# Kernel optimization log

Measured on AMD Instinct MI355X. Metric: run time of the kernel, lower is better.

Reference implementation:

```python
import jax, jax.numpy as jnp
import numpy as np

N_NODES = 50000
N_EDGES = 1600000
IN_DIM = 128
HID = 64
EPS = 1e-6


def setup_inputs() -> dict:
    key = jax.random.key(0)
    ks = jax.random.split(key, 12)
    def g(k, shape, scale):
        return jax.random.normal(k, shape, dtype=jnp.float32) * scale
    x = g(ks[0], (N_NODES, IN_DIM), 1.0)
    edge_index = jax.random.randint(ks[1], (2, N_EDGES), 0, N_NODES, dtype=jnp.int64)
    return {
        "x": x,
        "edge_index": edge_index,
        "w0s": g(ks[2], (IN_DIM, HID), 1.0 / np.sqrt(IN_DIM)),
        "w0n": g(ks[3], (IN_DIM, HID), 1.0 / np.sqrt(IN_DIM)),
        "w1s": g(ks[4], (HID, HID), 1.0 / np.sqrt(HID)),
        "w1n": g(ks[5], (HID, HID), 1.0 / np.sqrt(HID)),
        "w2s": g(ks[6], (HID, HID), 1.0 / np.sqrt(HID)),
        "w2n": g(ks[7], (HID, HID), 1.0 / np.sqrt(HID)),
        "mw1": g(ks[8], (HID, 32), 1.0 / np.sqrt(HID)),
        "mb1": jnp.zeros((32,), jnp.float32),
        "mw2": g(ks[9], (32, 1), 1.0 / np.sqrt(32.0)),
        "mb2": jnp.zeros((1,), jnp.float32),
    }


def _uhg_layer(h, src, dst, inv_deg, ws, wn):
    # transform-then-gather (cheaper: GEMM at node granularity, gather at edge granularity)
    msg = (h @ wn)[src]                                    # [E, HID]
    agg = jax.ops.segment_sum(msg, dst, num_segments=N_NODES) * inv_deg  # mean over in-neighbors
    h2 = jax.nn.relu(h @ ws + agg)
    # projective (UHG) normalization: map embedding back onto the unit sphere / projective rep
    return h2 / (jnp.linalg.norm(h2, axis=-1, keepdims=True) + EPS)


def reference(x, edge_index, w0s, w0n, w1s, w1n, w2s, w2n, mw1, mb1, mw2, mb2):
    src, dst = edge_index[0], edge_index[1]
    deg = jax.ops.segment_sum(jnp.ones((N_EDGES,), jnp.float32), dst, num_segments=N_NODES)
    inv_deg = (1.0 / jnp.maximum(deg, 1.0))[:, None]       # [N,1]
    h = _uhg_layer(x, src, dst, inv_deg, w0s, w0n)
    h = _uhg_layer(h, src, dst, inv_deg, w1s, w1n)
    h = _uhg_layer(h, src, dst, inv_deg, w2s, w2n)
    h = jax.nn.relu(h @ mw1 + mb1)                         # [N,32]
    return jax.nn.sigmoid(h @ mw2 + mb2)                   # [N,1]
```

## Files before the change

### kernel.cpp

```cpp
#include <hip/hip_runtime.h>
#include <hip/hip_bf16.h>
#include <math.h>

#define N_NODES 50000
#define N_EDGES 1600000
#define IN_DIM  128
#define HID     64
#define EPB     4096
#define NBLK    391
#define NB      391
#define CAP     8192
#define PBKT    8192
static constexpr float EPS = 1e-6f;

typedef __attribute__((ext_vector_type(8))) short          short8;
typedef __attribute__((ext_vector_type(8))) unsigned short ushort8;
typedef __attribute__((ext_vector_type(4))) unsigned short bf16x4_t;
typedef __attribute__((ext_vector_type(4))) int            i32x4;
typedef __attribute__((ext_vector_type(4))) float          f32x4;
typedef __attribute__((ext_vector_type(2))) float          f32x2;

__device__ __forceinline__ unsigned short f2bf(float f) {
    union { float f; unsigned int i; } c; c.f = f;
    unsigned int r = c.i + 0x7FFFu + ((c.i >> 16) & 1u);
    return (unsigned short)(r >> 16);
}
__device__ __forceinline__ unsigned char f2fp8(float f) {
    int p = __builtin_amdgcn_cvt_pk_fp8_f32(f, f, 0, false);
    return (unsigned char)(p & 0xff);
}


template <int K>
__device__ __forceinline__ void pack_body(const float* __restrict__ wS,
                                          const float* __restrict__ wN,
                                          unsigned short* __restrict__ pS,
                                          unsigned short* __restrict__ pN, int blk) {
    constexpr int NSLOT = (K / 32) * 4 * 64;
    int slot = blk * 256 + (int)threadIdx.x;
    if (slot >= NSLOT) return;
    int lane = slot & 63;
    int ct   = slot >> 6;
    int t    = ct & 3;
    int c    = ct >> 2;
    int m    = lane & 15;
    int quad = lane >> 4;
    int col  = t * 16 + m;
#pragma unroll
    for (int j = 0; j < 8; ++j) {
        int k = c * 32 + quad * 8 + j;
        pS[slot * 8 + j] = f2bf(wS[k * 64 + col]);
        pN[slot * 8 + j] = f2bf(wN[k * 64 + col]);
    }
}


__global__ __launch_bounds__(256) void bucket_count_pack(
    const int* __restrict__ ei, int* __restrict__ blockCounts,
    const float* __restrict__ w0s, const float* __restrict__ w0n,
    const float* __restrict__ w1s, const float* __restrict__ w1n,
    const float* __restrict__ w2s, const float* __restrict__ w2n,
    unsigned short* __restrict__ p0S, unsigned short* __restrict__ p0N,
    unsigned short* __restrict__ p1S, unsigned short* __restrict__ p1N,
    unsigned short* __restrict__ p2S, unsigned short* __restrict__ p2N,
    unsigned char* __restrict__ hnqA, unsigned char* __restrict__ hnqB) {
    if (blockIdx.x >= NBLK) {
        int blk = blockIdx.x - NBLK;
        if (blk == 7) {
            if (threadIdx.x >= 128 && threadIdx.x < 144)
                ((unsigned int*)(hnqA + (size_t)N_NODES * HID))[threadIdx.x - 128] = 0u;
            if (threadIdx.x >= 144 && threadIdx.x < 160)
                ((unsigned int*)(hnqB + (size_t)N_NODES * HID))[threadIdx.x - 144] = 0u;
        }
        if (blk < 4)      pack_body<IN_DIM>(w0s, w0n, p0S, p0N, blk);
        else if (blk < 6) pack_body<HID>(w1s, w1n, p1S, p1N, blk - 4);
        else              pack_body<HID>(w2s, w2n, p2S, p2N, blk - 6);
        return;
    }
    __shared__ int hist[NB];
    for (int i = threadIdx.x; i < NB; i += 256) hist[i] = 0;
    __syncthreads();
    int base = blockIdx.x * EPB;
    int lim  = min(EPB, N_EDGES - base);
    for (int i = threadIdx.x; i < lim; i += 256)
        atomicAdd(&hist[ei[N_EDGES + base + i] >> 7], 1);
    __syncthreads();
    for (int b = threadIdx.x; b < NB; b += 256)
        blockCounts[blockIdx.x * NB + b] = hist[b];
}

template <int K, bool F32IN>
__device__ __forceinline__ void gemm_body(
    const void* __restrict__ Av,
    const unsigned short* __restrict__ pS,
    const unsigned short* __restrict__ pN,
    float* __restrict__ hs, unsigned char* __restrict__ hnq, int blk) {
    constexpr int NC = K / 32;
    int lane = threadIdx.x & 63;
    int wv   = threadIdx.x >> 6;
    int tile = blk * 4 + wv;
    if (tile >= N_NODES / 16) return;
    int m    = lane & 15;
    int quad = lane >> 4;

    const short8* pSf = (const short8*)pS;
    const short8* pNf = (const short8*)pN;

    f32x4 accS[4], accN[4];
#pragma unroll
    for (int t = 0; t < 4; ++t) {
        accS[t] = (f32x4){0.f, 0.f, 0.f, 0.f};
        accN[t] = (f32x4){0.f, 0.f, 0.f, 0.f};
    }
#pragma unroll
    for (int c = 0; c < NC; ++c) {
        short8 a;
        if constexpr (F32IN) {
            const float* Af = (const float*)Av + ((size_t)tile * 16 + m) * K + quad * 8 + c * 32;
            f32x4 a0 = *(const f32x4*)Af;
            f32x4 a1 = *(const f32x4*)(Af + 4);
#pragma unroll
            for (int k = 0; k < 4; ++k) a[k]     = (short)f2bf(a0[k]);
#pragma unroll
            for (int k = 0; k < 4; ++k) a[k + 4] = (short)f2bf(a1[k]);
        } else {
            const short8* Af = (const short8*)((const unsigned short*)Av +
                               ((size_t)tile * 16 + m) * K + quad * 8);
            a = Af[c * 4];
        }
#pragma unroll
        for (int t = 0; t < 4; ++t) {
            short8 bs = pSf[(c * 4 + t) * 64 + lane];
            short8 bn = pNf[(c * 4 + t) * 64 + lane];
            accS[t] = __builtin_amdgcn_mfma_f32_16x16x32_bf16(a, bs, accS[t], 0, 0, 0);
            accN[t] = __builtin_amdgcn_mfma_f32_16x16x32_bf16(a, bn, accN[t], 0, 0, 0);
        }
    }
    int row0 = tile * 16 + quad * 4;
#pragma unroll
    for (int t = 0; t < 4; ++t) {
#pragma unroll
        for (int r = 0; r < 4; ++r) {
            size_t o = (size_t)(row0 + r) * HID + t * 16 + m;
            hs[o]  = accS[t][r];
            hnq[o] = f2fp8(accN[t][r]);
        }
    }
}

__global__ __launch_bounds__(256) void col_sum_gemm0(
    const int* __restrict__ blockCounts, int* __restrict__ totals,
    const float* __restrict__ x,
    const unsigned short* __restrict__ p0S, const unsigned short* __restrict__ p0N,
    float* __restrict__ hs, unsigned char* __restrict__ hnq) {
    if (blockIdx.x >= NB) {
        gemm_body<IN_DIM, true>(x, p0S, p0N, hs, hnq, blockIdx.x - NB);
        return;
    }
    __shared__ int ws[4];
    int b = blockIdx.x;
    int s = 0;
    for (int i = threadIdx.x; i < NBLK; i += 256) s += blockCounts[i * NB + b];
#pragma unroll
    for (int off = 32; off >= 1; off >>= 1) s += __shfl_xor(s, off, 64);
    if ((threadIdx.x & 63) == 0) ws[threadIdx.x >> 6] = s;
    __syncthreads();
    if (threadIdx.x == 0) totals[b] = ws[0] + ws[1] + ws[2] + ws[3];
}

__global__ __launch_bounds__(256) void col_fix_base(int* __restrict__ blockCounts,
                                                    const int* __restrict__ totals,
                                                    int* __restrict__ bucketBase) {
    __shared__ int vals[NBLK];
    __shared__ int sbase;
    int b = blockIdx.x;
    for (int i = threadIdx.x; i < NBLK; i += 256) vals[i] = blockCounts[i * NB + b];
    if (threadIdx.x < 64) {
        int lane = threadIdx.x;
        int s = 0;
        for (int i = lane; i < b; i += 64) s += totals[i];
#pragma unroll
        for (int off = 32; off >= 1; off >>= 1) s += __shfl_xor(s, off, 64);
        if (lane == 0) {
            sbase = s;
            bucketBase[b] = s;
            if (b == NB - 1) bucketBase[NB] = s + totals[b];
        }
    }
    __syncthreads();
    if (threadIdx.x < 64) {
        int lane  = threadIdx.x;
        int carry = sbase;
        for (int base = 0; base < NBLK; base += 64) {
            int i = base + lane;
            int v = (i < NBLK) ? vals[i] : 0;
            int incl = v;
#pragma unroll
            for (int off = 1; off < 64; off <<= 1) {
                int t = __shfl_up(incl, off, 64);
                if (lane >= off) incl += t;
            }
            if (i < NBLK) vals[i] = carry + incl - v;
            carry += __shfl(incl, 63, 64);
        }
    }
    __syncthreads();
    for (int i = threadIdx.x; i < NBLK; i += 256) blockCounts[i * NB + b] = vals[i];
}

__global__ __launch_bounds__(256) void bucket_scatter(const int* __restrict__ ei,
                                                      const int* __restrict__ blockCounts,
                                                      unsigned int* __restrict__ bucketPacked) {
    __shared__ int cur[NB];
    for (int b = threadIdx.x; b < NB; b += 256)
        cur[b] = blockCounts[blockIdx.x * NB + b];
    __syncthreads();
    int base = blockIdx.x * EPB;
    int lim  = min(EPB, N_EDGES - base);
    for (int i = threadIdx.x; i < lim; i += 256) {
        int s = ei[base + i];
        int d = ei[N_EDGES + base + i];
        int pos = atomicAdd(&cur[d >> 7], 1);
        bucketPacked[pos] = ((unsigned int)s << 7) | (unsigned int)(d & 127);
    }
}

__global__ __launch_bounds__(256) void node_scan_scatter_pad(
    const unsigned int* __restrict__ bucketPacked, const int* __restrict__ bucketBase,
    int* __restrict__ pbeg, int* __restrict__ rdeg, int* __restrict__ csr_pad) {
    __shared__ int cnt[128];
    __shared__ int half0;
    __shared__ unsigned int stage[CAP];
    int tid = threadIdx.x;
    if (tid < 128) cnt[tid] = 0;
    __syncthreads();
    int beg = bucketBase[blockIdx.x], end = bucketBase[blockIdx.x + 1];
    int n = end - beg;
    for (int i = tid; i < n; i += 256) {
        unsigned int e = bucketPacked[beg + i];
        if (i < CAP) stage[i] = e;
        atomicAdd(&cnt[e & 127], 1);
    }
    __syncthreads();
    int lane = tid & 63;
    int v    = (tid < 128) ? cnt[tid] : 0;
    int vp   = (v + 7) & ~7;
    int incl = vp;
#pragma unroll
    for (int off = 1; off < 64; off <<= 1) {
        int t = __shfl_up(incl, off, 64);
        if (lane >= off) incl += t;
    }
    if (tid == 63) half0 = incl;
    __syncthreads();
    int start = blockIdx.x * PBKT + ((tid >= 64 && tid < 128) ? half0 : 0) + incl - vp;
    int node  = blockIdx.x * 128 + tid;
    if (tid < 128 && node < N_NODES) {
        pbeg[node] = start;
        rdeg[node] = v;
        for (int j = v; j < vp; ++j) csr_pad[start + j] = N_NODES;
        cnt[tid] = start;
    }
    __syncthreads();
    for (int i = tid; i < n; i += 256) {
        unsigned int e = (i < CAP) ? stage[i] : bucketPacked[beg + i];
        int pos = atomicAdd(&cnt[e & 127], 1);
        csr_pad[pos] = (int)(e >> 7);
    }
}

template <bool MLP>
__global__ __launch_bounds__(256) void agg_update(
    const int* __restrict__ pbeg, const int* __restrict__ rdeg,
    const int* __restrict__ csr_pad,
    const unsigned char* __restrict__ hnq, const float* __restrict__ hs,
    const unsigned short* __restrict__ pS, const unsigned short* __restrict__ pN,
    float* __restrict__ hs2, unsigned char* __restrict__ hnq2,
    const float* __restrict__ mw1, const float* __restrict__ mb1,
    const float* __restrict__ mw2, const float* __restrict__ mb2,
    float* __restrict__ out) {
    __shared__ unsigned short sA[MLP ? 1 : 16 * 80];
    __shared__ float sW1[MLP ? HID * 32 : 1];
    __shared__ float sW2[MLP ? 32 : 1];
    __shared__ float sB1[MLP ? 32 : 1];
    __shared__ float sH[MLP ? 16 * 68 : 1];
    if (MLP) {
        for (int i = threadIdx.x; i < HID * 32; i += 256) sW1[i] = mw1[i];
        if (threadIdx.x < 32) { sW2[threadIdx.x] = mw2[threadIdx.x]; sB1[threadIdx.x] = mb1[threadIdx.x]; }
        __syncthreads();
    }
    int sn   = threadIdx.x >> 4;
    int r    = threadIdx.x & 15;
    int node = blockIdx.x * 16 + sn;
    int beg  = pbeg[node];
    int dg   = rdeg[node];
    int nbat = (dg + 7) >> 3;
    const i32x4* ip = (const i32x4*)(csr_pad + beg);
    unsigned r4 = (unsigned)(r * 4);

    f32x2 acc2[2];
    acc2[0] = (f32x2){0.f, 0.f};
    acc2[1] = (f32x2){0.f, 0.f};

#pragma unroll 2
    for (int t = 0; t < nbat; ++t) {
        i32x4 a = ip[2 * t];
        i32x4 b = ip[2 * t + 1];
        unsigned wv[8];
#pragma unroll
        for (int u = 0; u < 4; ++u)
            wv[u]     = *(const unsigned*)(hnq + (((unsigned)a[u] << 6) + r4));
#pragma unroll
        for (int u = 0; u < 4; ++u)
            wv[u + 4] = *(const unsigned*)(hnq + (((unsigned)b[u] << 6) + r4));
#pragma unroll
        for (int u = 0; u < 8; ++u) {
#if __has_builtin(__builtin_amdgcn_cvt_pk_f32_fp8)
            acc2[0] += __builtin_amdgcn_cvt_pk_f32_fp8((int)wv[u], false);
            acc2[1] += __builtin_amdgcn_cvt_pk_f32_fp8((int)wv[u], true);
#else
            acc2[0] += (f32x2){__builtin_amdgcn_cvt_f32_fp8((int)wv[u], 0),
                               __builtin_amdgcn_cvt_f32_fp8((int)wv[u], 1)};
            acc2[1] += (f32x2){__builtin_amdgcn_cvt_f32_fp8((int)wv[u], 2),
                               __builtin_amdgcn_cvt_f32_fp8((int)wv[u], 3)};
#endif
        }
    }

    float acc[4] = {acc2[0][0], acc2[0][1], acc2[1][0], acc2[1][1]};
    float invdeg = 1.0f / fmaxf((float)dg, 1.0f);
    f32x4 h = *(const f32x4*)(hs + (size_t)node * HID + r * 4);
    float v[4], ss = 0.f;
#pragma unroll
    for (int k = 0; k < 4; ++k) {
        v[k] = fmaxf(fmaf(acc[k], invdeg, h[k]), 0.f);
        ss += v[k] * v[k];
    }
    ss += __shfl_xor(ss, 1, 64);
    ss += __shfl_xor(ss, 2, 64);
    ss += __shfl_xor(ss, 4, 64);
    ss += __shfl_xor(ss, 8, 64);
    float rs = 1.0f / (sqrtf(ss) + EPS);

    if constexpr (!MLP) {
        unsigned short* ap = &sA[sn * 80 + r * 4];
#pragma unroll
        for (int k = 0; k < 4; ++k) ap[k] = f2bf(v[k] * rs);
        __syncthreads();
        int lane = threadIdx.x & 63;
        int wv_  = threadIdx.x >> 6;
        int m    = lane & 15;
        int quad = lane >> 4;
        const short8* pB = (const short8*)((wv_ < 2) ? pS : pN);
        int t0 = (wv_ & 1) * 2;
        f32x4 gacc[2];
        gacc[0] = (f32x4){0.f, 0.f, 0.f, 0.f};
        gacc[1] = (f32x4){0.f, 0.f, 0.f, 0.f};
#pragma unroll
        for (int c = 0; c < 2; ++c) {
            short8 a = *(const short8*)&sA[m * 80 + quad * 8 + c * 32];
#pragma unroll
            for (int tt = 0; tt < 2; ++tt) {
                short8 b = pB[(c * 4 + t0 + tt) * 64 + lane];
                gacc[tt] = __builtin_amdgcn_mfma_f32_16x16x32_bf16(a, b, gacc[tt], 0, 0, 0);
            }
        }
        int row0 = blockIdx.x * 16 + quad * 4;
#pragma unroll
        for (int tt = 0; tt < 2; ++tt) {
            int col = (t0 + tt) * 16 + m;
#pragma unroll
            for (int rr = 0; rr < 4; ++rr) {
                size_t o = (size_t)(row0 + rr) * HID + col;
                if (wv_ < 2) hs2[o]  = gacc[tt][rr];
                else         hnq2[o] = f2fp8(gacc[tt][rr]);
            }
        }
    } else {
#pragma unroll
        for (int k = 0; k < 4; ++k) sH[sn * 68 + r * 4 + k] = v[k] * rs;
        __syncthreads();
        int c0 = r * 2;
        float y0 = sB1[c0], y1 = sB1[c0 + 1];
        const float* hrow2 = &sH[sn * 68];
#pragma unroll 8
        for (int k = 0; k < HID; ++k) {
            float hv = hrow2[k];
            y0 = fmaf(hv, sW1[k * 32 + c0], y0);
            y1 = fmaf(hv, sW1[k * 32 + c0 + 1], y1);
        }
        float p = fmaxf(y0, 0.f) * sW2[c0] + fmaxf(y1, 0.f) * sW2[c0 + 1];
        p += __shfl_xor(p, 1, 64);
        p += __shfl_xor(p, 2, 64);
        p += __shfl_xor(p, 4, 64);
        p += __shfl_xor(p, 8, 64);
        if (r == 0) out[node] = 1.0f / (1.0f + __expf(-(p + mb2[0])));
    }
}

extern "C" void kernel_launch(void* const* d_in, const int* in_sizes, int n_in,
                              void* d_out, int out_size, void* d_ws, size_t ws_size,
                              hipStream_t stream) {
    const float* x   = (const float*)d_in[0];
    const int*   ei  = (const int*)d_in[1];
    const float* w0s = (const float*)d_in[2];
    const float* w0n = (const float*)d_in[3];
    const float* w1s = (const float*)d_in[4];
    const float* w1n = (const float*)d_in[5];
    const float* w2s = (const float*)d_in[6];
    const float* w2n = (const float*)d_in[7];
    const float* mw1 = (const float*)d_in[8];
    const float* mb1 = (const float*)d_in[9];
    const float* mw2 = (const float*)d_in[10];
    const float* mb2 = (const float*)d_in[11];
    float*       out = (float*)d_out;

    int* pbeg        = (int*)d_ws;
    int* rdeg        = pbeg + 50048;
    int* blockCounts = rdeg + 50048;
    int* bucketBase  = blockCounts + 153600;
    int* totals      = bucketBase + 512;
    unsigned int* bucketPacked = (unsigned int*)(totals + 512);
    int* csr_pad     = (int*)(bucketPacked + N_EDGES);
    const size_t NH = (size_t)N_NODES * HID;
    float*          hsA  = (float*)(csr_pad + NB * PBKT);
    unsigned char*  hnqA = (unsigned char*)(hsA + NH);
    float*          hsB  = (float*)(hnqA + NH + 64);
    unsigned char*  hnqB = (unsigned char*)(hsB + NH);
    unsigned short* p0S = (unsigned short*)(hnqB + NH + 64);
    unsigned short* p0N = p0S + IN_DIM * HID;
    unsigned short* p1S = p0N + IN_DIM * HID;
    unsigned short* p1N = p1S + HID * HID;
    unsigned short* p2S = p1N + HID * HID;
    unsigned short* p2N = p2S + HID * HID;

    const int nodeGrid = N_NODES / 16;
    const int gemmGrid = (N_NODES / 16 + 3) / 4;

    bucket_count_pack<<<NBLK + 8, 256, 0, stream>>>(
        ei, blockCounts, w0s, w0n, w1s, w1n, w2s, w2n,
        p0S, p0N, p1S, p1N, p2S, p2N, hnqA, hnqB);
    col_sum_gemm0<<<NB + gemmGrid, 256, 0, stream>>>(
        blockCounts, totals, x, p0S, p0N, hsA, hnqA);
    col_fix_base<<<NB, 256, 0, stream>>>(blockCounts, totals, bucketBase);
    bucket_scatter<<<NBLK, 256, 0, stream>>>(ei, blockCounts, bucketPacked);
    node_scan_scatter_pad<<<NB, 256, 0, stream>>>(bucketPacked, bucketBase,
                                                  pbeg, rdeg, csr_pad);

    agg_update<false><<<nodeGrid, 256, 0, stream>>>(
        pbeg, rdeg, csr_pad, hnqA, hsA, p1S, p1N, hsB, hnqB,
        nullptr, nullptr, nullptr, nullptr, nullptr);

    agg_update<false><<<nodeGrid, 256, 0, stream>>>(
        pbeg, rdeg, csr_pad, hnqB, hsB, p2S, p2N, hsA, hnqA,
        nullptr, nullptr, nullptr, nullptr, nullptr);

    agg_update<true><<<nodeGrid, 256, 0, stream>>>(
        pbeg, rdeg, csr_pad, hnqA, hsA, nullptr, nullptr, nullptr, nullptr,
        mw1, mb1, mw2, mb2, out);
}
```

Before: 204.1 us.

## Replace bucketed two-pass CSR build with global atomic degree count and scatter

Drops the per-block histogram, column scan, bucket scatter and per-bucket node scan kernels. Instead, per-node in-degrees are counted with global atomics, and a wave-level scan plus one atomic per wave allocates each node a padded CSR segment. Source indices are then scattered directly through per-node atomic cursors. This cuts the kernel count and the intermediate passes, at the cost of heavy global atomic contention and an edge order inside each row that is no longer deterministic. Row placement in memory becomes arbitrary because of the atomic segment allocation, which may hurt locality.

```diff
diff --git a/kernel.cpp b/kernel.cpp
--- a/kernel.cpp
+++ b/kernel.cpp
@@ -6,16 +6,11 @@
 #define N_EDGES 1600000
 #define IN_DIM  128
 #define HID     64
-#define EPB     4096
-#define NBLK    391
-#define NB      391
-#define CAP     8192
-#define PBKT    8192
+#define CBLK    1024
+#define SBLK    196
 static constexpr float EPS = 1e-6f;
 
 typedef __attribute__((ext_vector_type(8))) short          short8;
-typedef __attribute__((ext_vector_type(8))) unsigned short ushort8;
-typedef __attribute__((ext_vector_type(4))) unsigned short bf16x4_t;
 typedef __attribute__((ext_vector_type(4))) int            i32x4;
 typedef __attribute__((ext_vector_type(4))) float          f32x4;
 typedef __attribute__((ext_vector_type(2))) float          f32x2;
@@ -54,9 +49,13 @@
     }
 }
 
-
-__global__ __launch_bounds__(256) void bucket_count_pack(
-    const int* __restrict__ ei, int* __restrict__ blockCounts,
+__global__ __launch_bounds__(256) void zero_ws(int* __restrict__ z) {
+    int i = blockIdx.x * 256 + threadIdx.x;
+    if (i < 50112) z[i] = 0;
+}
+
+__global__ __launch_bounds__(256) void count_pack(
+    const int* __restrict__ ei, int* __restrict__ deg,
     const float* __restrict__ w0s, const float* __restrict__ w0n,
     const float* __restrict__ w1s, const float* __restrict__ w1n,
     const float* __restrict__ w2s, const float* __restrict__ w2n,
@@ -64,8 +63,8 @@
     unsigned short* __restrict__ p1S, unsigned short* __restrict__ p1N,
     unsigned short* __restrict__ p2S, unsigned short* __restrict__ p2N,
     unsigned char* __restrict__ hnqA, unsigned char* __restrict__ hnqB) {
-    if (blockIdx.x >= NBLK) {
-        int blk = blockIdx.x - NBLK;
+    if (blockIdx.x >= CBLK) {
+        int blk = blockIdx.x - CBLK;
         if (blk == 7) {
             if (threadIdx.x >= 128 && threadIdx.x < 144)
                 ((unsigned int*)(hnqA + (size_t)N_NODES * HID))[threadIdx.x - 128] = 0u;
@@ -77,16 +76,8 @@
         else              pack_body<HID>(w2s, w2n, p2S, p2N, blk - 6);
         return;
     }
-    __shared__ int hist[NB];
-    for (int i = threadIdx.x; i < NB; i += 256) hist[i] = 0;
-    __syncthreads();
-    int base = blockIdx.x * EPB;
-    int lim  = min(EPB, N_EDGES - base);
-    for (int i = threadIdx.x; i < lim; i += 256)
-        atomicAdd(&hist[ei[N_EDGES + base + i] >> 7], 1);
-    __syncthreads();
-    for (int b = threadIdx.x; b < NB; b += 256)
-        blockCounts[blockIdx.x * NB + b] = hist[b];
+    for (int i = blockIdx.x * 256 + threadIdx.x; i < N_EDGES; i += CBLK * 256)
+        atomicAdd(&deg[ei[N_EDGES + i]], 1);
 }
 
 template <int K, bool F32IN>
@@ -148,131 +139,52 @@
     }
 }
 
-__global__ __launch_bounds__(256) void col_sum_gemm0(
-    const int* __restrict__ blockCounts, int* __restrict__ totals,
+__global__ __launch_bounds__(256) void scan_gemm0(
+    const int* __restrict__ deg, int* __restrict__ pbeg, int* __restrict__ cursor,
+    int* __restrict__ csr, int* __restrict__ gcount,
     const float* __restrict__ x,
     const unsigned short* __restrict__ p0S, const unsigned short* __restrict__ p0N,
     float* __restrict__ hs, unsigned char* __restrict__ hnq) {
-    if (blockIdx.x >= NB) {
-        gemm_body<IN_DIM, true>(x, p0S, p0N, hs, hnq, blockIdx.x - NB);
+    if (blockIdx.x >= SBLK) {
+        gemm_body<IN_DIM, true>(x, p0S, p0N, hs, hnq, blockIdx.x - SBLK);
         return;
     }
-    __shared__ int ws[4];
-    int b = blockIdx.x;
-    int s = 0;
-    for (int i = threadIdx.x; i < NBLK; i += 256) s += blockCounts[i * NB + b];
-#pragma unroll
-    for (int off = 32; off >= 1; off >>= 1) s += __shfl_xor(s, off, 64);
-    if ((threadIdx.x & 63) == 0) ws[threadIdx.x >> 6] = s;
-    __syncthreads();
-    if (threadIdx.x == 0) totals[b] = ws[0] + ws[1] + ws[2] + ws[3];
-}
-
-__global__ __launch_bounds__(256) void col_fix_base(int* __restrict__ blockCounts,
-                                                    const int* __restrict__ totals,
-                                                    int* __restrict__ bucketBase) {
-    __shared__ int vals[NBLK];
-    __shared__ int sbase;
-    int b = blockIdx.x;
-    for (int i = threadIdx.x; i < NBLK; i += 256) vals[i] = blockCounts[i * NB + b];
-    if (threadIdx.x < 64) {
-        int lane = threadIdx.x;
-        int s = 0;
-        for (int i = lane; i < b; i += 64) s += totals[i];
-#pragma unroll
-        for (int off = 32; off >= 1; off >>= 1) s += __shfl_xor(s, off, 64);
-        if (lane == 0) {
-            sbase = s;
-            bucketBase[b] = s;
-            if (b == NB - 1) bucketBase[NB] = s + totals[b];
-        }
-    }
-    __syncthreads();
-    if (threadIdx.x < 64) {
-        int lane  = threadIdx.x;
-        int carry = sbase;
-        for (int base = 0; base < NBLK; base += 64) {
-            int i = base + lane;
-            int v = (i < NBLK) ? vals[i] : 0;
-            int incl = v;
-#pragma unroll
-            for (int off = 1; off < 64; off <<= 1) {
-                int t = __shfl_up(incl, off, 64);
-                if (lane >= off) incl += t;
-            }
-            if (i < NBLK) vals[i] = carry + incl - v;
-            carry += __shfl(incl, 63, 64);
-        }
-    }
-    __syncthreads();
-    for (int i = threadIdx.x; i < NBLK; i += 256) blockCounts[i * NB + b] = vals[i];
-}
-
-__global__ __launch_bounds__(256) void bucket_scatter(const int* __restrict__ ei,
-                                                      const int* __restrict__ blockCounts,
-                                                      unsigned int* __restrict__ bucketPacked) {
-    __shared__ int cur[NB];
-    for (int b = threadIdx.x; b < NB; b += 256)
-        cur[b] = blockCounts[blockIdx.x * NB + b];
-    __syncthreads();
-    int base = blockIdx.x * EPB;
-    int lim  = min(EPB, N_EDGES - base);
-    for (int i = threadIdx.x; i < lim; i += 256) {
-        int s = ei[base + i];
-        int d = ei[N_EDGES + base + i];
-        int pos = atomicAdd(&cur[d >> 7], 1);
-        bucketPacked[pos] = ((unsigned int)s << 7) | (unsigned int)(d & 127);
-    }
-}
-
-__global__ __launch_bounds__(256) void node_scan_scatter_pad(
-    const unsigned int* __restrict__ bucketPacked, const int* __restrict__ bucketBase,
-    int* __restrict__ pbeg, int* __restrict__ rdeg, int* __restrict__ csr_pad) {
-    __shared__ int cnt[128];
-    __shared__ int half0;
-    __shared__ unsigned int stage[CAP];
-    int tid = threadIdx.x;
-    if (tid < 128) cnt[tid] = 0;
-    __syncthreads();
-    int beg = bucketBase[blockIdx.x], end = bucketBase[blockIdx.x + 1];
-    int n = end - beg;
-    for (int i = tid; i < n; i += 256) {
-        unsigned int e = bucketPacked[beg + i];
-        if (i < CAP) stage[i] = e;
-        atomicAdd(&cnt[e & 127], 1);
-    }
-    __syncthreads();
-    int lane = tid & 63;
-    int v    = (tid < 128) ? cnt[tid] : 0;
-    int vp   = (v + 7) & ~7;
+    int node = blockIdx.x * 256 + threadIdx.x;
+    int lane = threadIdx.x & 63;
+    int d  = (node < N_NODES) ? deg[node] : 0;
+    int vp = (d + 7) & ~7;
     int incl = vp;
 #pragma unroll
     for (int off = 1; off < 64; off <<= 1) {
         int t = __shfl_up(incl, off, 64);
         if (lane >= off) incl += t;
     }
-    if (tid == 63) half0 = incl;
-    __syncthreads();
-    int start = blockIdx.x * PBKT + ((tid >= 64 && tid < 128) ? half0 : 0) + incl - vp;
-    int node  = blockIdx.x * 128 + tid;
-    if (tid < 128 && node < N_NODES) {
-        pbeg[node] = start;
-        rdeg[node] = v;
-        for (int j = v; j < vp; ++j) csr_pad[start + j] = N_NODES;
-        cnt[tid] = start;
-    }
-    __syncthreads();
-    for (int i = tid; i < n; i += 256) {
-        unsigned int e = (i < CAP) ? stage[i] : bucketPacked[beg + i];
-        int pos = atomicAdd(&cnt[e & 127], 1);
-        csr_pad[pos] = (int)(e >> 7);
+    int pos = 0;
+    if (lane == 63) pos = atomicAdd(gcount, incl);
+    pos = __shfl(pos, 63, 64);
+    int pb = pos + incl - vp;
+    if (node < N_NODES) {
+        pbeg[node]   = pb;
+        cursor[node] = pb;
+        for (int j = d; j < vp; ++j) csr[pb + j] = N_NODES;
+    }
+}
+
+__global__ __launch_bounds__(256) void scatter_csr(const int* __restrict__ ei,
+                                                   int* __restrict__ cursor,
+                                                   int* __restrict__ csr) {
+    for (int i = blockIdx.x * 256 + threadIdx.x; i < N_EDGES; i += CBLK * 256) {
+        int s = ei[i];
+        int d = ei[N_EDGES + i];
+        int pos = atomicAdd(&cursor[d], 1);
+        csr[pos] = s;
     }
 }
 
 template <bool MLP>
 __global__ __launch_bounds__(256) void agg_update(
     const int* __restrict__ pbeg, const int* __restrict__ rdeg,
-    const int* __restrict__ csr_pad,
+    const int* __restrict__ csr,
     const unsigned char* __restrict__ hnq, const float* __restrict__ hs,
     const unsigned short* __restrict__ pS, const unsigned short* __restrict__ pN,
     float* __restrict__ hs2, unsigned char* __restrict__ hnq2,
@@ -295,7 +207,7 @@
     int beg  = pbeg[node];
     int dg   = rdeg[node];
     int nbat = (dg + 7) >> 3;
-    const i32x4* ip = (const i32x4*)(csr_pad + beg);
+    const i32x4* ip = (const i32x4*)(csr + beg);
     unsigned r4 = (unsigned)(r * 4);
 
     f32x2 acc2[2];
@@ -415,15 +327,13 @@
     const float* mb2 = (const float*)d_in[11];
     float*       out = (float*)d_out;
 
-    int* pbeg        = (int*)d_ws;
-    int* rdeg        = pbeg + 50048;
-    int* blockCounts = rdeg + 50048;
-    int* bucketBase  = blockCounts + 153600;
-    int* totals      = bucketBase + 512;
-    unsigned int* bucketPacked = (unsigned int*)(totals + 512);
-    int* csr_pad     = (int*)(bucketPacked + N_EDGES);
+    int* deg     = (int*)d_ws;
+    int* gcount  = deg + 50048;
+    int* pbeg    = gcount + 64;
+    int* cursor  = pbeg + 50048;
+    int* csr     = cursor + 50048;
     const size_t NH = (size_t)N_NODES * HID;
-    float*          hsA  = (float*)(csr_pad + NB * PBKT);
+    float*          hsA  = (float*)(csr + 2000128);
     unsigned char*  hnqA = (unsigned char*)(hsA + NH);
     float*          hsB  = (float*)(hnqA + NH + 64);
     unsigned char*  hnqB = (unsigned char*)(hsB + NH);
@@ -434,28 +344,26 @@
     unsigned short* p2S = p1N + HID * HID;
     unsigned short* p2N = p2S + HID * HID;
 
-    const int nodeGrid = N_NODES / 16;
-    const int gemmGrid = (N_NODES / 16 + 3) / 4;
-
-    bucket_count_pack<<<NBLK + 8, 256, 0, stream>>>(
-        ei, blockCounts, w0s, w0n, w1s, w1n, w2s, w2n,
+    const int gemm0Grid = (N_NODES / 16 + 3) / 4;
+    const int nodeGrid  = N_NODES / 16;
+
+    zero_ws<<<SBLK + 1, 256, 0, stream>>>(deg);
+    count_pack<<<CBLK + 8, 256, 0, stream>>>(
+        ei, deg, w0s, w0n, w1s, w1n, w2s, w2n,
         p0S, p0N, p1S, p1N, p2S, p2N, hnqA, hnqB);
-    col_sum_gemm0<<<NB + gemmGrid, 256, 0, stream>>>(
-        blockCounts, totals, x, p0S, p0N, hsA, hnqA);
-    col_fix_base<<<NB, 256, 0, stream>>>(blockCounts, totals, bucketBase);
-    bucket_scatter<<<NBLK, 256, 0, stream>>>(ei, blockCounts, bucketPacked);
-    node_scan_scatter_pad<<<NB, 256, 0, stream>>>(bucketPacked, bucketBase,
-                                                  pbeg, rdeg, csr_pad);
+    scan_gemm0<<<SBLK + gemm0Grid, 256, 0, stream>>>(
+        deg, pbeg, cursor, csr, gcount, x, p0S, p0N, hsA, hnqA);
+    scatter_csr<<<CBLK, 256, 0, stream>>>(ei, cursor, csr);
 
     agg_update<false><<<nodeGrid, 256, 0, stream>>>(
-        pbeg, rdeg, csr_pad, hnqA, hsA, p1S, p1N, hsB, hnqB,
+        pbeg, deg, csr, hnqA, hsA, p1S, p1N, hsB, hnqB,
         nullptr, nullptr, nullptr, nullptr, nullptr);
 
     agg_update<false><<<nodeGrid, 256, 0, stream>>>(
-        pbeg, rdeg, csr_pad, hnqB, hsB, p2S, p2N, hsA, hnqA,
+        pbeg, deg, csr, hnqB, hsB, p2S, p2N, hsA, hnqA,
         nullptr, nullptr, nullptr, nullptr, nullptr);
 
     agg_update<true><<<nodeGrid, 256, 0, stream>>>(
-        pbeg, rdeg, csr_pad, hnqA, hsA, nullptr, nullptr, nullptr, nullptr,
+        pbeg, deg, csr, hnqA, hsA, nullptr, nullptr, nullptr, nullptr,
         mw1, mb1, mw2, mb2, out);
 }
```

Measured after the change: 360.3 us. 76.5% more time.
